# Kernel tuning notes

Measured on AMD Instinct MI355X. Metric: run time of the kernel, lower is better.

Reference implementation:

```python
import jax, jax.numpy as jnp
import numpy as np

B = 16384
TEXT_DIM = 768
IMAGE_DIM = 1024
HIDDEN = 1024
OUT_DIM = 1024
E = 8          # num_experts
K = 2          # top-k
NOISE_STD = 1.0
COMB = 2 * HIDDEN


def setup_inputs() -> dict:
    key = jax.random.key(0)
    ks = jax.random.split(key, 16)
    s = lambda d: 1.0 / np.sqrt(d)
    return {
        "text_emb": jax.random.normal(ks[0], (B, TEXT_DIM), jnp.float32),
        "image_emb": jax.random.normal(ks[1], (B, IMAGE_DIM), jnp.float32),
        "noise": jax.random.normal(ks[2], (B, E), jnp.float32),
        "Wt": jax.random.normal(ks[3], (TEXT_DIM, HIDDEN), jnp.float32) * s(TEXT_DIM),
        "bt": jnp.zeros((HIDDEN,), jnp.float32),
        "Wi": jax.random.normal(ks[4], (IMAGE_DIM, HIDDEN), jnp.float32) * s(IMAGE_DIM),
        "bi": jnp.zeros((HIDDEN,), jnp.float32),
        "Wg": jax.random.normal(ks[5], (COMB, E), jnp.float32) * s(COMB),
        "bg": jnp.zeros((E,), jnp.float32),
        "W1": jax.random.normal(ks[6], (E, COMB, HIDDEN), jnp.float32) * s(COMB),
        "b1": jnp.zeros((E, HIDDEN), jnp.float32),
        "W2": jax.random.normal(ks[7], (E, HIDDEN, OUT_DIM), jnp.float32) * s(HIDDEN),
        "b2": jnp.zeros((E, OUT_DIM), jnp.float32),
    }


def reference(text_emb, image_emb, noise, Wt, bt, Wi, bi, Wg, bg, W1, b1, W2, b2):
    # projections + concat -> combined [B, 2H]
    combined = jnp.concatenate([text_emb @ Wt + bt, image_emb @ Wi + bi], axis=-1)

    # noisy top-k gating
    clean_logits = combined @ Wg + bg            # [B, E]
    noisy_logits = clean_logits + noise * NOISE_STD
    topk_vals, topk_idx = jax.lax.top_k(noisy_logits, K)   # [B, K]
    topk_sm = jax.nn.softmax(topk_vals, axis=-1)
    rows = jnp.arange(combined.shape[0])[:, None]
    gate_weights = jnp.zeros_like(clean_logits).at[rows, topk_idx].set(topk_sm)  # [B, E]

    # run all experts densely (as in the original)
    h = jax.nn.relu(jnp.einsum('bd,edh->ebh', combined, W1) + b1[:, None, :])  # [E, B, H]
    out = jnp.einsum('ebh,eho->ebo', h, W2) + b2[:, None, :]                    # [E, B, O]

    # weighted sum over experts
    return jnp.einsum('be,ebo->bo', gate_weights, out)                          # [B, O]
```

## Files before the change

### kernel.cpp

```cpp
#include <hip/hip_runtime.h>
#include <stdint.h>
#include <stddef.h>

#define BB     16384
#define TD     768
#define ID_    1024
#define HID    1024
#define OD     1024
#define NE     8
#define CB     2048
#define CAPT   33792
#define GIN    1792

typedef __bf16 bf16;
typedef __bf16 bf16x4 __attribute__((ext_vector_type(4)));
typedef __bf16 bf16x8 __attribute__((ext_vector_type(8)));
typedef float  f32x4  __attribute__((ext_vector_type(4)));

struct Top2 { int e0, e1; float w0, w1; };
struct Slot2 { int p0, p1; };

__device__ __forceinline__ void gload16(void* lds, const void* g) {
#if __has_builtin(__builtin_amdgcn_global_load_lds)
  __builtin_amdgcn_global_load_lds(
      (const __attribute__((address_space(1))) void*)g,
      (__attribute__((address_space(3))) void*)lds, 16, 0, 0);
#else
  *(int4*)lds = *(const int4*)g;
#endif
}

__global__ void transpose_cvt(const float* __restrict__ src, bf16* __restrict__ dst,
                              int R, int C) {
  src += (size_t)blockIdx.z * R * C;
  dst += (size_t)blockIdx.z * R * C;
  __shared__ float tile[64][65];
  const int r0 = blockIdx.y * 64, c0 = blockIdx.x * 64;
  const int t = threadIdx.x;
#pragma unroll
  for (int i = 0; i < 16; ++i) {
    int e = i * 256 + t;
    int ii = e >> 6, jj = e & 63;
    tile[ii][jj] = src[(size_t)(r0 + ii) * C + (c0 + jj)];
  }
  __syncthreads();
#pragma unroll
  for (int i = 0; i < 16; ++i) {
    int e = i * 256 + t;
    int ii = e >> 6, jj = e & 63;
    dst[(size_t)(c0 + ii) * R + (r0 + jj)] = (bf16)tile[jj][ii];
  }
}

__global__ void fuse_w(const float* __restrict__ Wt, const float* __restrict__ Wi,
                       const float* __restrict__ Wg, const float* __restrict__ bt,
                       const float* __restrict__ bi, const float* __restrict__ bg,
                       double* __restrict__ WgF, double* __restrict__ bgd) {
  int o = blockIdx.x * blockDim.x + threadIdx.x;
  if (o >= (GIN + 1) * NE) return;
  int idx = o >> 3, e = o & 7;
  if (idx < TD) {
    double s = 0.0;
    for (int h = 0; h < HID; ++h)
      s += (double)Wt[(size_t)idx * HID + h] * (double)Wg[(size_t)h * NE + e];
    WgF[(size_t)e * GIN + idx] = s;
  } else if (idx < GIN) {
    int r = idx - TD;
    double s = 0.0;
    for (int h = 0; h < HID; ++h)
      s += (double)Wi[(size_t)r * HID + h] * (double)Wg[(size_t)(HID + h) * NE + e];
    WgF[(size_t)e * GIN + idx] = s;
  } else {
    double s = (double)bg[e];
    for (int h = 0; h < HID; ++h) {
      s += (double)bt[h] * (double)Wg[(size_t)h * NE + e];
      s += (double)bi[h] * (double)Wg[(size_t)(HID + h) * NE + e];
    }
    bgd[e] = s;
  }
}

__global__ __launch_bounds__(1024)
void route1(const float* __restrict__ text, const float* __restrict__ image,
            const float* __restrict__ noise,
            const double* __restrict__ WgF, const double* __restrict__ bgd,
            bf16* __restrict__ text_b, bf16* __restrict__ image_b,
            Top2* __restrict__ top2, int* __restrict__ counts) {
  __shared__ double wg[NE * GIN];
  __shared__ int lcnt[NE];
  const int t = threadIdx.x;
  if (t < NE) lcnt[t] = 0;
  {
    const ulonglong2* src = (const ulonglong2*)WgF;
    ulonglong2* dst = (ulonglong2*)wg;
#pragma unroll
    for (int i = 0; i < (NE * GIN) / 2 / 1024; ++i)
      dst[i * 1024 + t] = src[i * 1024 + t];
  }
  __syncthreads();

  const int wave = t >> 6, lane = t & 63;
  const int row0 = blockIdx.x * 64;
#pragma unroll
  for (int rr = 0; rr < 4; ++rr) {
    const int row = row0 + wave + rr * 16;
    const float* tr = text + (size_t)row * TD;
    const float* ir = image + (size_t)row * ID_;
    float xv[28];
#pragma unroll
    for (int c = 0; c < 12; ++c) xv[c] = tr[lane + 64 * c];
#pragma unroll
    for (int c = 0; c < 16; ++c) xv[12 + c] = ir[lane + 64 * c];
    bf16* tb = text_b + (size_t)row * TD;
    bf16* ib = image_b + (size_t)row * ID_;
#pragma unroll
    for (int c = 0; c < 12; ++c) tb[lane + 64 * c] = (bf16)xv[c];
#pragma unroll
    for (int c = 0; c < 16; ++c) ib[lane + 64 * c] = (bf16)xv[12 + c];

    double acc[NE];
#pragma unroll
    for (int e = 0; e < NE; ++e) acc[e] = 0.0;
#pragma unroll
    for (int c = 0; c < 28; ++c) {
      const double vd = (double)xv[c];
      const int idx = lane + 64 * c;
#pragma unroll
      for (int e = 0; e < NE; ++e) acc[e] = fma(vd, wg[e * GIN + idx], acc[e]);
    }
#pragma unroll
    for (int off = 32; off > 0; off >>= 1) {
#pragma unroll
      for (int e = 0; e < NE; ++e) acc[e] += __shfl_down(acc[e], off);
    }
    if (lane == 0) {
      float nz[NE];
#pragma unroll
      for (int e = 0; e < NE; ++e)
        nz[e] = (float)(acc[e] + bgd[e]) + noise[(size_t)row * NE + e];
      int i0 = 0;
#pragma unroll
      for (int e = 1; e < NE; ++e) if (nz[e] > nz[i0]) i0 = e;
      int i1 = (i0 == 0) ? 1 : 0;
#pragma unroll
      for (int e = 0; e < NE; ++e) if (e != i0 && nz[e] > nz[i1]) i1 = e;
      float tt = expf(nz[i1] - nz[i0]);
      float w0 = 1.0f / (1.0f + tt);
      float w1 = tt / (1.0f + tt);
      Top2 rec; rec.e0 = i0; rec.e1 = i1; rec.w0 = w0; rec.w1 = w1;
      top2[row] = rec;
      atomicAdd(&lcnt[i0], 1);
      atomicAdd(&lcnt[i1], 1);
    }
  }
  __syncthreads();
  if (t < NE) atomicAdd(&counts[t], lcnt[t]);
}

__global__ void scan_pad(const int* __restrict__ counts, int* __restrict__ offsets,
                         int* __restrict__ padded, int* __restrict__ pos,
                         int* __restrict__ rows_list, float* __restrict__ wgt_list) {
  __shared__ int s_off[NE], s_cnt[NE], s_pad[NE];
  if (threadIdx.x == 0) {
    int off = 0;
    for (int e = 0; e < NE; ++e) {
      int c = counts[e];
      int pd = (c + 127) & ~127;
      s_cnt[e] = c; s_pad[e] = pd; s_off[e] = off;
      offsets[e] = off; padded[e] = pd; pos[e] = off;
      off += pd;
    }
    offsets[NE] = off;
  }
  __syncthreads();
  for (int e = 0; e < NE; ++e) {
    for (int i = s_cnt[e] + threadIdx.x; i < s_pad[e]; i += blockDim.x) {
      rows_list[s_off[e] + i] = 0;
      wgt_list[s_off[e] + i] = 0.0f;
    }
  }
}

__global__ void route2(const Top2* __restrict__ top2, int* __restrict__ pos,
                       int* __restrict__ rows_list, float* __restrict__ wgt_list,
                       Slot2* __restrict__ slots) {
  __shared__ int lcnt[NE], lbase[NE];
  if (threadIdx.x < NE) lcnt[threadIdx.x] = 0;
  __syncthreads();
  const int r = blockIdx.x * 256 + threadIdx.x;
  Top2 tt = top2[r];
  int s0 = atomicAdd(&lcnt[tt.e0], 1);
  int s1 = atomicAdd(&lcnt[tt.e1], 1);
  __syncthreads();
  if (threadIdx.x < NE)
    lbase[threadIdx.x] = atomicAdd(&pos[threadIdx.x], lcnt[threadIdx.x]);
  __syncthreads();
  int p0 = lbase[tt.e0] + s0;
  rows_list[p0] = r; wgt_list[p0] = tt.w0;
  int p1 = lbase[tt.e1] + s1;
  rows_list[p1] = r; wgt_list[p1] = tt.w1;
  Slot2 sl; sl.p0 = p0; sl.p1 = p1;
  slots[r] = sl;
}

__global__ __launch_bounds__(256)
void combine(const bf16* __restrict__ pairb, const Slot2* __restrict__ slots,
             float* __restrict__ out) {
  const int row = blockIdx.x;
  const Slot2 s = slots[row];
  const int t = threadIdx.x;
  const bf16x4 a = *(const bf16x4*)(pairb + (size_t)s.p0 * OD + t * 4);
  const bf16x4 b = *(const bf16x4*)(pairb + (size_t)s.p1 * OD + t * 4);
  f32x4 r;
#pragma unroll
  for (int j = 0; j < 4; ++j) r[j] = (float)a[j] + (float)b[j];
  *(f32x4*)(out + (size_t)row * OD + t * 4) = r;
}


#define BARe  do { __builtin_amdgcn_s_barrier(); __builtin_amdgcn_sched_barrier(0); } while (0)
#define LGKM0 do { asm volatile("s_waitcnt lgkmcnt(0)" ::: "memory"); \
                   __builtin_amdgcn_sched_barrier(0); } while (0)
#define VMC4  asm volatile("s_waitcnt vmcnt(4)" ::: "memory")
#define PRIO1 __builtin_amdgcn_s_setprio(1)
#define PRIO0 __builtin_amdgcn_s_setprio(0)

#define STAGE128(BUF, KT) do { \
  _Pragma("unroll") for (int j_ = 0; j_ < 2; ++j_) { \
    gload16(&As[BUF][ldsoff[j_]], aptr[j_] + (size_t)(KT) * 32); \
    gload16(&Bs[BUF][ldsoff[j_]], bptr[j_] + (size_t)(KT) * 32); \
  } \
} while (0)

template<int MODE>
__global__ __launch_bounds__(256, 4)
void gemm128(const bf16* __restrict__ A, const bf16* __restrict__ BT,
             const float* __restrict__ bias, bf16* __restrict__ outb,
             const int* __restrict__ rows_list, const float* __restrict__ wgt_list,
             const int* __restrict__ offsets, const int* __restrict__ padded,
             int K, int lda, int ldb, int ldout, int coloff) {
  __shared__ bf16 As[2][128 * 32];
  __shared__ bf16 Bs[2][128 * 32];
  const int t = threadIdx.x;
  const int lane = t & 63, w = t >> 6;
  const int wm = w >> 1, wn = w & 1;
  const int bid = blockIdx.x;
  const int xcd = bid & 7, sdec = bid >> 3;
  const int nblk = sdec & 7, mblk = (sdec >> 3) * 8 + xcd;

  long base = 0;
  if constexpr (MODE != 0) {
    const int e = blockIdx.z;
    if (mblk * 128 >= padded[e]) return;
    base = offsets[e];
    if constexpr (MODE == 1) { BT += (size_t)e * HID * CB; bias += e * HID; }
    else                     { BT += (size_t)e * OD * HID; bias += e * OD; }
  }

  const bf16* aptr[2]; const bf16* bptr[2]; int ldsoff[2];
#pragma unroll
  for (int j = 0; j < 2; ++j) {
    const int g = j * 256 + t, row = g >> 2;
    const int scol = ((g & 3) ^ ((row >> 1) & 3)) * 8;
    long ga;
    if constexpr (MODE == 1)      ga = rows_list[base + (long)mblk * 128 + row];
    else if constexpr (MODE == 2) ga = base + (long)mblk * 128 + row;
    else                          ga = (long)mblk * 128 + row;
    aptr[j] = A + ga * lda + scol;
    bptr[j] = BT + (size_t)(nblk * 128 + row) * ldb + scol;
    ldsoff[j] = g * 8;
  }

  const int fr = lane & 15;
  const int swz = ((lane >> 4) ^ ((fr >> 1) & 3)) * 8;
  int a_off[4], b_off[4];
#pragma unroll
  for (int f = 0; f < 4; ++f) {
    a_off[f] = (wm * 64 + f * 16 + fr) * 32 + swz;
    b_off[f] = (wn * 64 + f * 16 + fr) * 32 + swz;
  }

  f32x4 acc[4][4];
#pragma unroll
  for (int i = 0; i < 4; ++i)
#pragma unroll
    for (int j = 0; j < 4; ++j)
#pragma unroll
      for (int r = 0; r < 4; ++r) acc[i][j][r] = 0.0f;

  const int NKT = K >> 5;

  STAGE128(0, 0);
  for (int kt = 0; kt < NKT; ++kt) {
    const int kn = (kt + 1 < NKT) ? kt + 1 : 0;
    BARe;
    STAGE128((kt + 1) & 1, kn);
    VMC4;
    BARe;
    bf16x8 af[4], bfr[4];
#pragma unroll
    for (int f = 0; f < 4; ++f) af[f]  = *(const bf16x8*)(&As[kt & 1][a_off[f]]);
#pragma unroll
    for (int f = 0; f < 4; ++f) bfr[f] = *(const bf16x8*)(&Bs[kt & 1][b_off[f]]);
    LGKM0;
    PRIO1;
#pragma unroll
    for (int mf = 0; mf < 4; ++mf)
#pragma unroll
      for (int nf = 0; nf < 4; ++nf)
        acc[mf][nf] = __builtin_amdgcn_mfma_f32_16x16x32_bf16(af[mf], bfr[nf],
                                                              acc[mf][nf], 0, 0, 0);
    PRIO0;
  }

  const int row_h = (lane >> 4) * 4;
#pragma unroll
  for (int nf = 0; nf < 4; ++nf) {
    const int gcol = nblk * 128 + wn * 64 + nf * 16 + fr;
    const float bv = bias[gcol];
#pragma unroll
    for (int mf = 0; mf < 4; ++mf) {
      const int rbase = wm * 64 + mf * 16 + row_h;
#pragma unroll
      for (int r = 0; r < 4; ++r) {
        const int rit = rbase + r;
        float v = acc[mf][nf][r] + bv;
        if constexpr (MODE == 0) {
          outb[((size_t)mblk * 128 + rit) * ldout + coloff + gcol] = (bf16)v;
        } else if constexpr (MODE == 1) {
          outb[(size_t)(base + (long)mblk * 128 + rit) * ldout + gcol] =
              (bf16)fmaxf(v, 0.0f);
        } else {
          const long li = base + (long)mblk * 128 + rit;
          const float wgt = wgt_list[li];
          outb[(size_t)li * ldout + gcol] = (bf16)(wgt * v);
        }
      }
    }
  }
}

extern "C" void kernel_launch(void* const* d_in, const int* in_sizes, int n_in,
                              void* d_out, int out_size, void* d_ws, size_t ws_size,
                              hipStream_t stream) {
  const float* text  = (const float*)d_in[0];
  const float* image = (const float*)d_in[1];
  const float* noise = (const float*)d_in[2];
  const float* Wt    = (const float*)d_in[3];
  const float* bt    = (const float*)d_in[4];
  const float* Wi    = (const float*)d_in[5];
  const float* bi    = (const float*)d_in[6];
  const float* Wg    = (const float*)d_in[7];
  const float* bg    = (const float*)d_in[8];
  const float* W1    = (const float*)d_in[9];
  const float* b1    = (const float*)d_in[10];
  const float* W2    = (const float*)d_in[11];
  const float* b2    = (const float*)d_in[12];
  float* out = (float*)d_out;

  char* p = (char*)d_ws;
  auto alloc = [&](size_t bytes) {
    char* r = p; p += (bytes + 255) & ~(size_t)255; return r;
  };
  const size_t sz_text  = (size_t)BB * TD * 2;
  const size_t sz_texta = (sz_text + 255) & ~(size_t)255;
  const size_t sz_image = (size_t)BB * ID_ * 2;
  const size_t sz_pair  = (size_t)CAPT * OD * 2;
  size_t sz_u0 = sz_texta + sz_image;
  if (sz_pair > sz_u0) sz_u0 = sz_pair;
  char* u0 = alloc(sz_u0);
  bf16* text_b  = (bf16*)u0;
  bf16* image_b = (bf16*)(u0 + sz_texta);
  bf16* pairb   = (bf16*)u0;

  bf16*   WtT      = (bf16*)alloc((size_t)HID * TD * 2);
  bf16*   WiT      = (bf16*)alloc((size_t)HID * ID_ * 2);
  bf16*   W1T      = (bf16*)alloc((size_t)NE * HID * CB * 2);
  bf16*   W2T      = (bf16*)alloc((size_t)NE * OD * HID * 2);
  bf16*   combined = (bf16*)alloc((size_t)BB * CB * 2);
  bf16*   hbuf     = (bf16*)alloc((size_t)CAPT * HID * 2);
  double* WgF      = (double*)alloc((size_t)NE * GIN * 8);
  double* bgd      = (double*)alloc((size_t)NE * 8);
  Top2*   top2     = (Top2*)alloc((size_t)BB * sizeof(Top2));
  Slot2*  slots    = (Slot2*)alloc((size_t)BB * sizeof(Slot2));
  int*    counts   = (int*)alloc(NE * 4);
  int*    offsets  = (int*)alloc((NE + 1) * 4);
  int*    padded   = (int*)alloc(NE * 4);
  int*    pos      = (int*)alloc(NE * 4);
  int*    rows_list= (int*)alloc((size_t)CAPT * 4);
  float*  wgt_list = (float*)alloc((size_t)CAPT * 4);

  hipMemsetAsync(counts, 0, NE * 4, stream);

  transpose_cvt<<<dim3(HID / 64, TD / 64, 1),  256, 0, stream>>>(Wt, WtT, TD, HID);
  transpose_cvt<<<dim3(HID / 64, ID_ / 64, 1), 256, 0, stream>>>(Wi, WiT, ID_, HID);
  transpose_cvt<<<dim3(HID / 64, CB / 64, NE), 256, 0, stream>>>(W1, W1T, CB, HID);
  transpose_cvt<<<dim3(OD / 64, HID / 64, NE), 256, 0, stream>>>(W2, W2T, HID, OD);

  fuse_w<<<((GIN + 1) * NE + 255) / 256, 256, 0, stream>>>(
      Wt, Wi, Wg, bt, bi, bg, WgF, bgd);
  route1<<<BB / 64, 1024, 0, stream>>>(text, image, noise, WgF, bgd,
                                       text_b, image_b, top2, counts);
  scan_pad<<<1, 256, 0, stream>>>(counts, offsets, padded, pos, rows_list, wgt_list);
  route2<<<BB / 256, 256, 0, stream>>>(top2, pos, rows_list, wgt_list, slots);

  gemm128<0><<<dim3(1024, 1, 1), 256, 0, stream>>>(
      text_b, WtT, bt, combined, nullptr, nullptr, nullptr, nullptr,
      TD, TD, TD, CB, 0);
  gemm128<0><<<dim3(1024, 1, 1), 256, 0, stream>>>(
      image_b, WiT, bi, combined, nullptr, nullptr, nullptr, nullptr,
      ID_, ID_, ID_, CB, HID);
  gemm128<1><<<dim3(1024, 1, NE), 256, 0, stream>>>(
      combined, W1T, b1, hbuf, rows_list, nullptr, offsets, padded,
      CB, CB, CB, HID, 0);
  gemm128<2><<<dim3(1024, 1, NE), 256, 0, stream>>>(
      hbuf, W2T, b2, pairb, rows_list, wgt_list, offsets, padded,
      HID, HID, HID, OD, 0);
  combine<<<BB, 256, 0, stream>>>(pairb, slots, out);
}
```

Baseline: 574.2 us.

## Enlarge GEMM tiles to 256x128 with triple-buffered LDS pipeline

Changes all GEMMs from 128x128 tiles to 256x128 tiles, with each wave computing 128x64 (8x4 MFMA fragments), and pads expert segments to multiples of 256. It also switches to a three-stage LDS buffer that prefetches two k-steps ahead, waiting with vmcnt(12). The aim is more reuse of B operands per load and better hiding of global-load latency. In exchange it uses more registers and LDS (occupancy hint drops from 4 to 2 blocks), adds more padding waste per expert, and launches fewer blocks.

```diff
diff --git a/kernel.cpp b/kernel.cpp
--- a/kernel.cpp
+++ b/kernel.cpp
@@ -9,7 +9,7 @@
 #define OD     1024
 #define NE     8
 #define CB     2048
-#define CAPT   33792
+#define CAPT   34816
 #define GIN    1792
 
 typedef __bf16 bf16;
@@ -165,7 +165,7 @@
     int off = 0;
     for (int e = 0; e < NE; ++e) {
       int c = counts[e];
-      int pd = (c + 127) & ~127;
+      int pd = (c + 255) & ~255;
       s_cnt[e] = c; s_pad[e] = pd; s_off[e] = off;
       offsets[e] = off; padded[e] = pd; pos[e] = off;
       off += pd;
@@ -221,26 +221,26 @@
 #define BARe  do { __builtin_amdgcn_s_barrier(); __builtin_amdgcn_sched_barrier(0); } while (0)
 #define LGKM0 do { asm volatile("s_waitcnt lgkmcnt(0)" ::: "memory"); \
                    __builtin_amdgcn_sched_barrier(0); } while (0)
-#define VMC4  asm volatile("s_waitcnt vmcnt(4)" ::: "memory")
+#define VMC12 asm volatile("s_waitcnt vmcnt(12)" ::: "memory")
 #define PRIO1 __builtin_amdgcn_s_setprio(1)
 #define PRIO0 __builtin_amdgcn_s_setprio(0)
 
-#define STAGE128(BUF, KT) do { \
-  _Pragma("unroll") for (int j_ = 0; j_ < 2; ++j_) { \
-    gload16(&As[BUF][ldsoff[j_]], aptr[j_] + (size_t)(KT) * 32); \
-    gload16(&Bs[BUF][ldsoff[j_]], bptr[j_] + (size_t)(KT) * 32); \
-  } \
+#define STAGE_AB(BUF, KT) do { \
+  _Pragma("unroll") for (int j_ = 0; j_ < 4; ++j_) \
+    gload16(&As[BUF][aldso[j_]], aptr[j_] + (size_t)(KT) * 32); \
+  _Pragma("unroll") for (int j_ = 0; j_ < 2; ++j_) \
+    gload16(&Bs[BUF][bldso[j_]], bptr[j_] + (size_t)(KT) * 32); \
 } while (0)
 
 template<int MODE>
-__global__ __launch_bounds__(256, 4)
-void gemm128(const bf16* __restrict__ A, const bf16* __restrict__ BT,
-             const float* __restrict__ bias, bf16* __restrict__ outb,
-             const int* __restrict__ rows_list, const float* __restrict__ wgt_list,
-             const int* __restrict__ offsets, const int* __restrict__ padded,
-             int K, int lda, int ldb, int ldout, int coloff) {
-  __shared__ bf16 As[2][128 * 32];
-  __shared__ bf16 Bs[2][128 * 32];
+__global__ __launch_bounds__(256, 2)
+void gemm256x128(const bf16* __restrict__ A, const bf16* __restrict__ BT,
+                 const float* __restrict__ bias, bf16* __restrict__ outb,
+                 const int* __restrict__ rows_list, const float* __restrict__ wgt_list,
+                 const int* __restrict__ offsets, const int* __restrict__ padded,
+                 int K, int lda, int ldb, int ldout, int coloff) {
+  __shared__ bf16 As[3][256 * 32];
+  __shared__ bf16 Bs[3][128 * 32];
   const int t = threadIdx.x;
   const int lane = t & 63, w = t >> 6;
   const int wm = w >> 1, wn = w & 1;
@@ -251,38 +251,44 @@
   long base = 0;
   if constexpr (MODE != 0) {
     const int e = blockIdx.z;
-    if (mblk * 128 >= padded[e]) return;
+    if (mblk * 256 >= padded[e]) return;
     base = offsets[e];
     if constexpr (MODE == 1) { BT += (size_t)e * HID * CB; bias += e * HID; }
     else                     { BT += (size_t)e * OD * HID; bias += e * OD; }
   }
 
-  const bf16* aptr[2]; const bf16* bptr[2]; int ldsoff[2];
+  const bf16* aptr[4]; int aldso[4];
+#pragma unroll
+  for (int j = 0; j < 4; ++j) {
+    const int g = j * 256 + t, row = g >> 2;
+    const int scol = ((g & 3) ^ ((row >> 1) & 3)) * 8;
+    long ga;
+    if constexpr (MODE == 1)      ga = rows_list[base + (long)mblk * 256 + row];
+    else if constexpr (MODE == 2) ga = base + (long)mblk * 256 + row;
+    else                          ga = (long)mblk * 256 + row;
+    aptr[j] = A + ga * lda + scol;
+    aldso[j] = g * 8;
+  }
+  const bf16* bptr[2]; int bldso[2];
 #pragma unroll
   for (int j = 0; j < 2; ++j) {
     const int g = j * 256 + t, row = g >> 2;
     const int scol = ((g & 3) ^ ((row >> 1) & 3)) * 8;
-    long ga;
-    if constexpr (MODE == 1)      ga = rows_list[base + (long)mblk * 128 + row];
-    else if constexpr (MODE == 2) ga = base + (long)mblk * 128 + row;
-    else                          ga = (long)mblk * 128 + row;
-    aptr[j] = A + ga * lda + scol;
     bptr[j] = BT + (size_t)(nblk * 128 + row) * ldb + scol;
-    ldsoff[j] = g * 8;
+    bldso[j] = g * 8;
   }
 
   const int fr = lane & 15;
   const int swz = ((lane >> 4) ^ ((fr >> 1) & 3)) * 8;
-  int a_off[4], b_off[4];
-#pragma unroll
-  for (int f = 0; f < 4; ++f) {
-    a_off[f] = (wm * 64 + f * 16 + fr) * 32 + swz;
-    b_off[f] = (wn * 64 + f * 16 + fr) * 32 + swz;
-  }
-
-  f32x4 acc[4][4];
-#pragma unroll
-  for (int i = 0; i < 4; ++i)
+  int a_off[8], b_off[4];
+#pragma unroll
+  for (int f = 0; f < 8; ++f) a_off[f] = (wm * 128 + f * 16 + fr) * 32 + swz;
+#pragma unroll
+  for (int f = 0; f < 4; ++f) b_off[f] = (wn * 64 + f * 16 + fr) * 32 + swz;
+
+  f32x4 acc[8][4];
+#pragma unroll
+  for (int i = 0; i < 8; ++i)
 #pragma unroll
     for (int j = 0; j < 4; ++j)
 #pragma unroll
@@ -290,27 +296,31 @@
 
   const int NKT = K >> 5;
 
-  STAGE128(0, 0);
+  STAGE_AB(0, 0);
+  STAGE_AB(1, 1);
+  int cur = 0;
   for (int kt = 0; kt < NKT; ++kt) {
-    const int kn = (kt + 1 < NKT) ? kt + 1 : 0;
+    const int kn = (kt + 2 < NKT) ? kt + 2 : 0;
+    int sn = cur + 2; if (sn >= 3) sn -= 3;
     BARe;
-    STAGE128((kt + 1) & 1, kn);
-    VMC4;
+    STAGE_AB(sn, kn);
+    VMC12;
     BARe;
-    bf16x8 af[4], bfr[4];
-#pragma unroll
-    for (int f = 0; f < 4; ++f) af[f]  = *(const bf16x8*)(&As[kt & 1][a_off[f]]);
-#pragma unroll
-    for (int f = 0; f < 4; ++f) bfr[f] = *(const bf16x8*)(&Bs[kt & 1][b_off[f]]);
+    bf16x8 af[8], bfr[4];
+#pragma unroll
+    for (int f = 0; f < 8; ++f) af[f]  = *(const bf16x8*)(&As[cur][a_off[f]]);
+#pragma unroll
+    for (int f = 0; f < 4; ++f) bfr[f] = *(const bf16x8*)(&Bs[cur][b_off[f]]);
     LGKM0;
     PRIO1;
 #pragma unroll
-    for (int mf = 0; mf < 4; ++mf)
+    for (int mf = 0; mf < 8; ++mf)
 #pragma unroll
       for (int nf = 0; nf < 4; ++nf)
         acc[mf][nf] = __builtin_amdgcn_mfma_f32_16x16x32_bf16(af[mf], bfr[nf],
                                                               acc[mf][nf], 0, 0, 0);
     PRIO0;
+    cur = (cur + 1 < 3) ? cur + 1 : 0;
   }
 
   const int row_h = (lane >> 4) * 4;
@@ -319,19 +329,19 @@
     const int gcol = nblk * 128 + wn * 64 + nf * 16 + fr;
     const float bv = bias[gcol];
 #pragma unroll
-    for (int mf = 0; mf < 4; ++mf) {
-      const int rbase = wm * 64 + mf * 16 + row_h;
+    for (int mf = 0; mf < 8; ++mf) {
+      const int rbase = wm * 128 + mf * 16 + row_h;
 #pragma unroll
       for (int r = 0; r < 4; ++r) {
         const int rit = rbase + r;
         float v = acc[mf][nf][r] + bv;
         if constexpr (MODE == 0) {
-          outb[((size_t)mblk * 128 + rit) * ldout + coloff + gcol] = (bf16)v;
+          outb[((size_t)mblk * 256 + rit) * ldout + coloff + gcol] = (bf16)v;
         } else if constexpr (MODE == 1) {
-          outb[(size_t)(base + (long)mblk * 128 + rit) * ldout + gcol] =
+          outb[(size_t)(base + (long)mblk * 256 + rit) * ldout + gcol] =
               (bf16)fmaxf(v, 0.0f);
         } else {
-          const long li = base + (long)mblk * 128 + rit;
+          const long li = base + (long)mblk * 256 + rit;
           const float wgt = wgt_list[li];
           outb[(size_t)li * ldout + gcol] = (bf16)(wgt * v);
         }
@@ -404,16 +414,16 @@
   scan_pad<<<1, 256, 0, stream>>>(counts, offsets, padded, pos, rows_list, wgt_list);
   route2<<<BB / 256, 256, 0, stream>>>(top2, pos, rows_list, wgt_list, slots);
 
-  gemm128<0><<<dim3(1024, 1, 1), 256, 0, stream>>>(
+  gemm256x128<0><<<dim3(512, 1, 1), 256, 0, stream>>>(
       text_b, WtT, bt, combined, nullptr, nullptr, nullptr, nullptr,
       TD, TD, TD, CB, 0);
-  gemm128<0><<<dim3(1024, 1, 1), 256, 0, stream>>>(
+  gemm256x128<0><<<dim3(512, 1, 1), 256, 0, stream>>>(
       image_b, WiT, bi, combined, nullptr, nullptr, nullptr, nullptr,
       ID_, ID_, ID_, CB, HID);
-  gemm128<1><<<dim3(1024, 1, NE), 256, 0, stream>>>(
+  gemm256x128<1><<<dim3(512, 1, NE), 256, 0, stream>>>(
       combined, W1T, b1, hbuf, rows_list, nullptr, offsets, padded,
       CB, CB, CB, HID, 0);
-  gemm128<2><<<dim3(1024, 1, NE), 256, 0, stream>>>(
+  gemm256x128<2><<<dim3(512, 1, NE), 256, 0, stream>>>(
       hbuf, W2T, b2, pairb, rows_list, wgt_list, offsets, padded,
       HID, HID, HID, OD, 0);
   combine<<<BB, 256, 0, stream>>>(pairb, slots, out);
```

Result: slower. 650.6 us (+13.3%).

## Switch gemm128 to single-buffered K=64 tiles with wider swizzle

Applied to the files above, without the earlier changes.

The GEMM main loop changes from double-buffered 32-wide K tiles to a single 64-wide K tile per iteration, with an 8-way XOR swizzle and two MFMA sub-steps per tile. This halves the number of barriers per K and keeps the LDS footprint the same. The cost is that global loads are no longer overlapped with compute: the loop waits on vmcnt(0) before each tile and issues the next stage only after the MFMAs finish. It relies on the 4 blocks per CU to hide that load latency.

```diff
diff --git a/kernel.cpp b/kernel.cpp
--- a/kernel.cpp
+++ b/kernel.cpp
@@ -219,16 +219,14 @@
 
 
 #define BARe  do { __builtin_amdgcn_s_barrier(); __builtin_amdgcn_sched_barrier(0); } while (0)
-#define LGKM0 do { asm volatile("s_waitcnt lgkmcnt(0)" ::: "memory"); \
-                   __builtin_amdgcn_sched_barrier(0); } while (0)
-#define VMC4  asm volatile("s_waitcnt vmcnt(4)" ::: "memory")
+#define VMC0  asm volatile("s_waitcnt vmcnt(0)" ::: "memory")
 #define PRIO1 __builtin_amdgcn_s_setprio(1)
 #define PRIO0 __builtin_amdgcn_s_setprio(0)
 
-#define STAGE128(BUF, KT) do { \
-  _Pragma("unroll") for (int j_ = 0; j_ < 2; ++j_) { \
-    gload16(&As[BUF][ldsoff[j_]], aptr[j_] + (size_t)(KT) * 32); \
-    gload16(&Bs[BUF][ldsoff[j_]], bptr[j_] + (size_t)(KT) * 32); \
+#define STAGE64(KT) do { \
+  _Pragma("unroll") for (int j_ = 0; j_ < 4; ++j_) { \
+    gload16(&As[ldso[j_]], aptr[j_] + (size_t)(KT) * 64); \
+    gload16(&Bs[ldso[j_]], bptr[j_] + (size_t)(KT) * 64); \
   } \
 } while (0)
 
@@ -239,8 +237,8 @@
              const int* __restrict__ rows_list, const float* __restrict__ wgt_list,
              const int* __restrict__ offsets, const int* __restrict__ padded,
              int K, int lda, int ldb, int ldout, int coloff) {
-  __shared__ bf16 As[2][128 * 32];
-  __shared__ bf16 Bs[2][128 * 32];
+  __shared__ bf16 As[128 * 64];
+  __shared__ bf16 Bs[128 * 64];
   const int t = threadIdx.x;
   const int lane = t & 63, w = t >> 6;
   const int wm = w >> 1, wn = w & 1;
@@ -257,27 +255,27 @@
     else                     { BT += (size_t)e * OD * HID; bias += e * OD; }
   }
 
-  const bf16* aptr[2]; const bf16* bptr[2]; int ldsoff[2];
-#pragma unroll
-  for (int j = 0; j < 2; ++j) {
-    const int g = j * 256 + t, row = g >> 2;
-    const int scol = ((g & 3) ^ ((row >> 1) & 3)) * 8;
+  const int scol = ((t & 7) ^ ((t >> 3) & 7)) * 8;
+  const bf16* aptr[4]; const bf16* bptr[4]; int ldso[4];
+#pragma unroll
+  for (int j = 0; j < 4; ++j) {
+    const int row = j * 32 + (t >> 3);
     long ga;
     if constexpr (MODE == 1)      ga = rows_list[base + (long)mblk * 128 + row];
     else if constexpr (MODE == 2) ga = base + (long)mblk * 128 + row;
     else                          ga = (long)mblk * 128 + row;
     aptr[j] = A + ga * lda + scol;
     bptr[j] = BT + (size_t)(nblk * 128 + row) * ldb + scol;
-    ldsoff[j] = g * 8;
-  }
-
-  const int fr = lane & 15;
-  const int swz = ((lane >> 4) ^ ((fr >> 1) & 3)) * 8;
+    ldso[j] = (j * 256 + t) * 8;
+  }
+
+  const int fr = lane & 15, hi = lane >> 4;
+  const int rsw = hi ^ (fr & 7);
   int a_off[4], b_off[4];
 #pragma unroll
   for (int f = 0; f < 4; ++f) {
-    a_off[f] = (wm * 64 + f * 16 + fr) * 32 + swz;
-    b_off[f] = (wn * 64 + f * 16 + fr) * 32 + swz;
+    a_off[f] = ((wm * 64 + f * 16 + fr) * 8 + rsw) * 8;
+    b_off[f] = ((wn * 64 + f * 16 + fr) * 8 + rsw) * 8;
   }
 
   f32x4 acc[4][4];
@@ -288,32 +286,33 @@
 #pragma unroll
       for (int r = 0; r < 4; ++r) acc[i][j][r] = 0.0f;
 
-  const int NKT = K >> 5;
-
-  STAGE128(0, 0);
+  const int NKT = K >> 6;
+
+  STAGE64(0);
   for (int kt = 0; kt < NKT; ++kt) {
-    const int kn = (kt + 1 < NKT) ? kt + 1 : 0;
+    VMC0;
     BARe;
-    STAGE128((kt + 1) & 1, kn);
-    VMC4;
+#pragma unroll
+    for (int kk = 0; kk < 2; ++kk) {
+      bf16x8 af[4], bfr[4];
+#pragma unroll
+      for (int f = 0; f < 4; ++f) af[f]  = *(const bf16x8*)(&As[a_off[f] ^ (kk * 32)]);
+#pragma unroll
+      for (int f = 0; f < 4; ++f) bfr[f] = *(const bf16x8*)(&Bs[b_off[f] ^ (kk * 32)]);
+      PRIO1;
+#pragma unroll
+      for (int mf = 0; mf < 4; ++mf)
+#pragma unroll
+        for (int nf = 0; nf < 4; ++nf)
+          acc[mf][nf] = __builtin_amdgcn_mfma_f32_16x16x32_bf16(af[mf], bfr[nf],
+                                                                acc[mf][nf], 0, 0, 0);
+      PRIO0;
+    }
     BARe;
-    bf16x8 af[4], bfr[4];
-#pragma unroll
-    for (int f = 0; f < 4; ++f) af[f]  = *(const bf16x8*)(&As[kt & 1][a_off[f]]);
-#pragma unroll
-    for (int f = 0; f < 4; ++f) bfr[f] = *(const bf16x8*)(&Bs[kt & 1][b_off[f]]);
-    LGKM0;
-    PRIO1;
-#pragma unroll
-    for (int mf = 0; mf < 4; ++mf)
-#pragma unroll
-      for (int nf = 0; nf < 4; ++nf)
-        acc[mf][nf] = __builtin_amdgcn_mfma_f32_16x16x32_bf16(af[mf], bfr[nf],
-                                                              acc[mf][nf], 0, 0, 0);
-    PRIO0;
-  }
-
-  const int row_h = (lane >> 4) * 4;
+    if (kt + 1 < NKT) STAGE64(kt + 1);
+  }
+
+  const int row_h = hi * 4;
 #pragma unroll
   for (int nf = 0; nf < 4; ++nf) {
     const int gcol = nblk * 128 + wn * 64 + nf * 16 + fr;
```

New measurement: 528.7 us. 7.9% less time.
